# Kernel tuning notes

Measured on AMD Instinct MI355X. Metric: run time of the kernel, lower is better.

The kernel has to match this reference:

```python
import jax, jax.numpy as jnp
import numpy as np

WS = 7           # window size
N = WS * WS      # tokens per window = 49
C = 128          # embed dim
H = 4            # heads
HD = C // H      # head dim = 32
NW = 64          # num windows (mask leading dim)
B = 4096         # total windows = outer_batch * NW


def _relative_indexes():
    ch = np.arange(WS)
    cw = np.arange(WS)
    coords = np.stack(np.meshgrid(ch, cw, indexing='ij')).reshape(2, -1)  # [2, N]
    rel = coords[:, :, None] - coords[:, None, :]                          # [2, N, N]
    rel = rel.transpose(1, 2, 0)
    rel[:, :, 0] += WS - 1
    rel[:, :, 1] += WS - 1
    rel[:, :, 0] *= 2 * WS - 1
    return jnp.asarray(rel.sum(-1), dtype=jnp.int32)                       # [N, N]


def setup_inputs() -> dict:
    key = jax.random.key(0)
    ks = jax.random.split(key, 10)
    s = 0.02
    return {
        'query': jax.random.normal(ks[0], (B, N, C), jnp.float32),
        'source': jax.random.normal(ks[1], (B, N, C), jnp.float32),
        'mask': jnp.zeros((NW, N, N), jnp.float32),
        'q_w': jax.random.normal(ks[2], (C, C), jnp.float32) * s,
        'q_b': jnp.zeros((C,), jnp.float32),
        'kv_w': jax.random.normal(ks[3], (C, 2 * C), jnp.float32) * s,
        'kv_b': jnp.zeros((2 * C,), jnp.float32),
        'proj_w': jax.random.normal(ks[4], (C, C), jnp.float32) * s,
        'proj_b': jnp.zeros((C,), jnp.float32),
        'bias_table': jax.random.normal(ks[5], ((2 * WS - 1) ** 2, H), jnp.float32) * s,
        'rel_idx': _relative_indexes(),
    }


def reference(query, source, mask, q_w, q_b, kv_w, kv_b, proj_w, proj_b, bias_table, rel_idx):
    scale = HD ** -0.5
    q = query @ q_w + q_b                       # [B, N, C]
    kv = source @ kv_w + kv_b                   # [B, N, 2C]
    k, v = kv[..., :C], kv[..., C:]
    # [B, N, H, HD] -> [B, H, N, HD]
    q = q.reshape(B, N, H, HD).transpose(0, 2, 1, 3) * scale
    k = k.reshape(B, N, H, HD).transpose(0, 2, 1, 3)
    v = v.reshape(B, N, H, HD).transpose(0, 2, 1, 3)
    attn = jnp.einsum('bhnd,bhmd->bhnm', q, k)  # [B, H, N, N]
    # gathered relative positional bias: [1, H, N, N]
    bias = bias_table[rel_idx.reshape(-1)].reshape(N, N, H).transpose(2, 0, 1)[None]
    attn = attn + bias
    # mask: [NW, N, N] broadcast over outer batch and heads
    attn = attn.reshape(-1, NW, H, N, N) + mask[None, :, None]
    attn = attn.reshape(B, H, N, N)
    attn = jax.nn.softmax(attn, axis=-1)
    x = jnp.einsum('bhnm,bhmd->bnhd', attn, v).reshape(B, N, C)
    return x @ proj_w + proj_b
```

## Files before the change

kernel.cpp:

```cpp
#include <hip/hip_runtime.h>
#include <hip/hip_bf16.h>

#define NN 49
#define CC 128
#define HH 4
#define NWIN 64
#define BB 4096
#define QSCALE 0.17677669529663687f

typedef __attribute__((ext_vector_type(8))) short bf16x8;
typedef __attribute__((ext_vector_type(4))) float f32x4;
typedef unsigned short u16;
typedef unsigned int u32;

__device__ __forceinline__ u16 f2b(float f) {
    __hip_bfloat16 h = __float2bfloat16(f);
    return __builtin_bit_cast(u16, h);
}
__device__ __forceinline__ float b2f(u16 u) { return __uint_as_float(((u32)u) << 16); }
__device__ __forceinline__ uint2 pack4(float a, float b, float c, float d) {
    uint2 r;
    r.x = (u32)f2b(a) | ((u32)f2b(b) << 16);
    r.y = (u32)f2b(c) | ((u32)f2b(d) << 16);
    return r;
}
__device__ __forceinline__ f32x4 mfma16(bf16x8 a, bf16x8 b, f32x4 c) {
    return __builtin_amdgcn_mfma_f32_16x16x32_bf16(a, b, c, 0, 0, 0);
}
__device__ __forceinline__ char* adr256(u16* base, int row, int byte) {
    return (char*)base + row * 256 + (byte ^ ((row & 7) << 4));
}
__device__ __forceinline__ char* adr128(u16* base, int row, int byte) {
    return (char*)base + row * 128 + (byte ^ ((row & 7) << 4));
}

__global__ void prep_cbt(const float* __restrict__ bias_table, const int* __restrict__ rel_idx,
                         const float* __restrict__ mask, u16* __restrict__ cbt) {
    int idx = blockIdx.x * blockDim.x + threadIdx.x;
    int m = idx & 63, i = (idx >> 6) & 63, h = (idx >> 12) & 3, wv = idx >> 14;
    if (wv >= NWIN) return;
    float v = -1e9f;
    if (m < NN && i < NN)
        v = bias_table[rel_idx[i * NN + m] * HH + h] + mask[(wv * NN + i) * NN + m];
    cbt[idx] = f2b(v);
}

__global__ void prep_w(const float* __restrict__ qw, const float* __restrict__ qb,
                       const float* __restrict__ kvw, const float* __restrict__ pjw,
                       u16* __restrict__ qwp, u16* __restrict__ kvwp,
                       u16* __restrict__ pjwp, float* __restrict__ qbs) {
    int idx = blockIdx.x * blockDim.x + threadIdx.x;
    if (idx < 16384) {
        int i = idx & 7, lane = (idx >> 3) & 63, kt = (idx >> 9) & 3, nt = idx >> 11;
        int k = 32 * kt + 8 * (lane >> 4) + i, n = 16 * nt + (lane & 15);
        qwp[idx] = f2b(qw[k * CC + n] * QSCALE);
    } else if (idx < 49152) {
        int j = idx - 16384;
        int i = j & 7, lane = (j >> 3) & 63, kt = (j >> 9) & 3, nt = j >> 11;
        int k = 32 * kt + 8 * (lane >> 4) + i, n = 16 * nt + (lane & 15);
        kvwp[j] = f2b(kvw[k * 2 * CC + n]);
    } else if (idx < 65536) {
        int j = idx - 49152;
        int i = j & 7, lane = (j >> 3) & 63, kt = (j >> 9) & 3, nt = j >> 11;
        int k = 32 * kt + 8 * (lane >> 4) + i, n = 16 * nt + (lane & 15);
        pjwp[j] = f2b(pjw[k * CC + n]);
    } else if (idx < 65664) {
        int j = idx - 65536;
        qbs[j] = qb[j] * QSCALE;
    }
}

__global__ __launch_bounds__(512, 4)
void wmha_main(const float* __restrict__ query, const float* __restrict__ source,
               const u16* __restrict__ qwp, const u16* __restrict__ kvwp,
               const u16* __restrict__ pjwp, const float* __restrict__ qbs,
               const float* __restrict__ kv_b, const float* __restrict__ proj_b,
               const u16* __restrict__ cbt, float* __restrict__ out) {
    __shared__ u16 lds[24576];
    u16* R0 = lds;
    u16* R1 = lds + 8192;
    u16* R2 = lds + 16384;
    const int t = threadIdx.x;
    const int b = blockIdx.x;
    const int w = t >> 6, lane = t & 63;
    const int lq = lane & 15, qd = lane >> 4;
    const int mw = w >> 2;
    const int nw = w & 3;
    const int h = w >> 1;
    const int half = w & 1;

    {
        const int row = t >> 3, qu = t & 7;
        const size_t gbase = (size_t)b * NN * CC + row * CC + qu * 8;
        #pragma unroll
        for (int j = 0; j < 2; ++j) {
            bf16x8 vq = {0,0,0,0,0,0,0,0}, vs = {0,0,0,0,0,0,0,0};
            if (row < NN) {
                const float4* q4 = (const float4*)(query + gbase) + 16 * j;
                const float4* s4 = (const float4*)(source + gbase) + 16 * j;
                float4 a0 = q4[0], a1 = q4[1], c0 = s4[0], c1 = s4[1];
                vq[0]=(short)f2b(a0.x); vq[1]=(short)f2b(a0.y); vq[2]=(short)f2b(a0.z); vq[3]=(short)f2b(a0.w);
                vq[4]=(short)f2b(a1.x); vq[5]=(short)f2b(a1.y); vq[6]=(short)f2b(a1.z); vq[7]=(short)f2b(a1.w);
                vs[0]=(short)f2b(c0.x); vs[1]=(short)f2b(c0.y); vs[2]=(short)f2b(c0.z); vs[3]=(short)f2b(c0.w);
                vs[4]=(short)f2b(c1.x); vs[5]=(short)f2b(c1.y); vs[6]=(short)f2b(c1.z); vs[7]=(short)f2b(c1.w);
            }
            *(bf16x8*)adr256(R0, row, qu * 16 + 128 * j) = vq;
            *(bf16x8*)adr256(R2, row, qu * 16 + 128 * j) = vs;
        }
    }
    bf16x8 bwq[2][4];
    #pragma unroll
    for (int n2 = 0; n2 < 2; ++n2)
        #pragma unroll
        for (int kt = 0; kt < 4; ++kt)
            bwq[n2][kt] = *(const bf16x8*)(qwp + (((nw + 4 * n2) * 4 + kt) * 64 + lane) * 8);
    __syncthreads();

    {
        bf16x8 a[2][4];
        #pragma unroll
        for (int m2 = 0; m2 < 2; ++m2)
            #pragma unroll
            for (int kt = 0; kt < 4; ++kt)
                a[m2][kt] = *(const bf16x8*)adr256(R0, (2 * mw + m2) * 16 + lq, kt * 64 + qd * 16);
        f32x4 acc[2][2] = {};
        __builtin_amdgcn_s_setprio(1);
        #pragma unroll
        for (int m2 = 0; m2 < 2; ++m2)
            #pragma unroll
            for (int n2 = 0; n2 < 2; ++n2)
                #pragma unroll
                for (int kt = 0; kt < 4; ++kt)
                    acc[m2][n2] = mfma16(a[m2][kt], bwq[n2][kt], acc[m2][n2]);
        __builtin_amdgcn_s_setprio(0);
        #pragma unroll
        for (int n2 = 0; n2 < 2; ++n2) {
            const int col = 16 * (nw + 4 * n2) + lq;
            const float bias = qbs[col];
            #pragma unroll
            for (int m2 = 0; m2 < 2; ++m2)
                #pragma unroll
                for (int r = 0; r < 4; ++r) {
                    const int row = (2 * mw + m2) * 16 + qd * 4 + r;
                    *(u16*)adr256(R1, row, 2 * col) = f2b(acc[m2][n2][r] + bias);
                }
        }
    }
    __syncthreads();

    {
        bf16x8 bw[2][4];
        #pragma unroll
        for (int n2 = 0; n2 < 2; ++n2)
            #pragma unroll
            for (int kt = 0; kt < 4; ++kt)
                bw[n2][kt] = *(const bf16x8*)(kvwp + (((nw + 4 * n2) * 4 + kt) * 64 + lane) * 8);
        bf16x8 a[2][4];
        #pragma unroll
        for (int m2 = 0; m2 < 2; ++m2)
            #pragma unroll
            for (int kt = 0; kt < 4; ++kt)
                a[m2][kt] = *(const bf16x8*)adr256(R2, (2 * mw + m2) * 16 + lq, kt * 64 + qd * 16);
        f32x4 acc[2][2] = {};
        __builtin_amdgcn_s_setprio(1);
        #pragma unroll
        for (int m2 = 0; m2 < 2; ++m2)
            #pragma unroll
            for (int n2 = 0; n2 < 2; ++n2)
                #pragma unroll
                for (int kt = 0; kt < 4; ++kt)
                    acc[m2][n2] = mfma16(a[m2][kt], bw[n2][kt], acc[m2][n2]);
        __builtin_amdgcn_s_setprio(0);
        #pragma unroll
        for (int n2 = 0; n2 < 2; ++n2) {
            const int col = 16 * (nw + 4 * n2) + lq;
            const float bias = kv_b[col];
            #pragma unroll
            for (int m2 = 0; m2 < 2; ++m2)
                #pragma unroll
                for (int r = 0; r < 4; ++r) {
                    const int row = (2 * mw + m2) * 16 + qd * 4 + r;
                    *(u16*)adr256(R0, row, 2 * col) = f2b(acc[m2][n2][r] + bias);
                }
        }
    }

    {
        bf16x8 bw[2][4];
        #pragma unroll
        for (int n2 = 0; n2 < 2; ++n2)
            #pragma unroll
            for (int kt = 0; kt < 4; ++kt)
                bw[n2][kt] = *(const bf16x8*)(kvwp + (((8 + nw + 4 * n2) * 4 + kt) * 64 + lane) * 8);
        bf16x8 a[2][4];
        #pragma unroll
        for (int m2 = 0; m2 < 2; ++m2)
            #pragma unroll
            for (int kt = 0; kt < 4; ++kt)
                a[m2][kt] = *(const bf16x8*)adr256(R2, (2 * mw + m2) * 16 + lq, kt * 64 + qd * 16);
        f32x4 acc[2][2] = {};
        __builtin_amdgcn_s_setprio(1);
        #pragma unroll
        for (int m2 = 0; m2 < 2; ++m2)
            #pragma unroll
            for (int n2 = 0; n2 < 2; ++n2)
                #pragma unroll
                for (int kt = 0; kt < 4; ++kt)
                    acc[m2][n2] = mfma16(a[m2][kt], bw[n2][kt], acc[m2][n2]);
        __builtin_amdgcn_s_setprio(0);
        __syncthreads();
        #pragma unroll
        for (int n2 = 0; n2 < 2; ++n2) {
            const int dim = 16 * (nw + 4 * n2) + lq;
            const float bias = kv_b[CC + dim];
            #pragma unroll
            for (int m2 = 0; m2 < 2; ++m2) {
                uint2 pk = pack4(acc[m2][n2][0] + bias, acc[m2][n2][1] + bias,
                                 acc[m2][n2][2] + bias, acc[m2][n2][3] + bias);
                *(uint2*)adr128(R2, dim, 2 * ((2 * mw + m2) * 16 + qd * 4)) = pk;
            }
        }
    }

    f32x4 s[2][4];
    {
        bf16x8 kf[4], qf[2];
        #pragma unroll
        for (int a = 0; a < 4; ++a)
            kf[a] = *(const bf16x8*)adr256(R0, a * 16 + lq, h * 64 + qd * 16);
        #pragma unroll
        for (int i = 0; i < 2; ++i)
            qf[i] = *(const bf16x8*)adr256(R1, (2 * half + i) * 16 + lq, h * 64 + qd * 16);
        __builtin_amdgcn_s_setprio(1);
        #pragma unroll
        for (int i = 0; i < 2; ++i) {
            f32x4 z = {0.f, 0.f, 0.f, 0.f};
            #pragma unroll
            for (int a = 0; a < 4; ++a)
                s[i][a] = mfma16(kf[a], qf[i], z);
        }
        __builtin_amdgcn_s_setprio(0);
    }
    __syncthreads();

    {
        bf16x8 vf[2][2];
        #pragma unroll
        for (int dt = 0; dt < 2; ++dt)
            #pragma unroll
            for (int kt = 0; kt < 2; ++kt)
                vf[dt][kt] = *(const bf16x8*)adr128(R2, h * 32 + dt * 16 + lq, kt * 64 + qd * 16);
        u16* pb = R0 + w * 1024;
        const u16* cbb = cbt + ((size_t)((b & (NWIN - 1)) * HH + h) << 12);
        #pragma unroll
        for (int i = 0; i < 2; ++i) {
            const int bq = 2 * half + i;
            uint2 cb2[4];
            #pragma unroll
            for (int a = 0; a < 4; ++a)
                cb2[a] = *(const uint2*)(cbb + (bq * 16 + lq) * 64 + a * 16 + qd * 4);
            #pragma unroll
            for (int a = 0; a < 4; ++a) {
                s[i][a][0] += b2f((u16)(cb2[a].x & 0xffffu));
                s[i][a][1] += b2f((u16)(cb2[a].x >> 16));
                s[i][a][2] += b2f((u16)(cb2[a].y & 0xffffu));
                s[i][a][3] += b2f((u16)(cb2[a].y >> 16));
            }
            float m0 = s[i][0][0];
            #pragma unroll
            for (int a = 0; a < 4; ++a)
                #pragma unroll
                for (int r = 0; r < 4; ++r) m0 = fmaxf(m0, s[i][a][r]);
            m0 = fmaxf(m0, __shfl_xor(m0, 16));
            m0 = fmaxf(m0, __shfl_xor(m0, 32));
            uint2 pk[4];
            float sm = 0.f;
            #pragma unroll
            for (int a = 0; a < 4; ++a) {
                float p0 = __expf(s[i][a][0] - m0), p1 = __expf(s[i][a][1] - m0);
                float p2 = __expf(s[i][a][2] - m0), p3 = __expf(s[i][a][3] - m0);
                pk[a] = pack4(p0, p1, p2, p3);
                sm += b2f((u16)pk[a].x) + b2f((u16)(pk[a].x >> 16))
                    + b2f((u16)pk[a].y) + b2f((u16)(pk[a].y >> 16));
            }
            sm += __shfl_xor(sm, 16);
            sm += __shfl_xor(sm, 32);
            const float inv = 1.f / sm;
            #pragma unroll
            for (int a = 0; a < 4; ++a)
                *(uint2*)adr128(pb, lq, 32 * a + 8 * qd) = pk[a];
            asm volatile("s_waitcnt lgkmcnt(0)" ::: "memory");
            __builtin_amdgcn_sched_barrier(0);
            f32x4 o[2] = {{0.f,0.f,0.f,0.f},{0.f,0.f,0.f,0.f}};
            __builtin_amdgcn_s_setprio(1);
            #pragma unroll
            for (int kt = 0; kt < 2; ++kt) {
                bf16x8 pf = *(const bf16x8*)adr128(pb, lq, 64 * kt + 16 * qd);
                #pragma unroll
                for (int dt = 0; dt < 2; ++dt)
                    o[dt] = mfma16(vf[dt][kt], pf, o[dt]);
            }
            __builtin_amdgcn_s_setprio(0);
            __builtin_amdgcn_sched_barrier(0);
            #pragma unroll
            for (int dt = 0; dt < 2; ++dt) {
                uint2 px = pack4(o[dt][0] * inv, o[dt][1] * inv,
                                 o[dt][2] * inv, o[dt][3] * inv);
                *(uint2*)adr256(R1, bq * 16 + lq, 64 * h + 32 * dt + 8 * qd) = px;
            }
        }
    }

    {
        bf16x8 bw[2][4];
        #pragma unroll
        for (int n2 = 0; n2 < 2; ++n2)
            #pragma unroll
            for (int kt = 0; kt < 4; ++kt)
                bw[n2][kt] = *(const bf16x8*)(pjwp + (((nw + 4 * n2) * 4 + kt) * 64 + lane) * 8);
        __syncthreads();
        bf16x8 a[2][4];
        #pragma unroll
        for (int m2 = 0; m2 < 2; ++m2)
            #pragma unroll
            for (int kt = 0; kt < 4; ++kt)
                a[m2][kt] = *(const bf16x8*)adr256(R1, (2 * mw + m2) * 16 + lq, kt * 64 + qd * 16);
        f32x4 acc[2][2] = {};
        __builtin_amdgcn_s_setprio(1);
        #pragma unroll
        for (int m2 = 0; m2 < 2; ++m2)
            #pragma unroll
            for (int n2 = 0; n2 < 2; ++n2)
                #pragma unroll
                for (int kt = 0; kt < 4; ++kt)
                    acc[m2][n2] = mfma16(a[m2][kt], bw[n2][kt], acc[m2][n2]);
        __builtin_amdgcn_s_setprio(0);
        float* outb = out + (size_t)b * NN * CC;
        #pragma unroll
        for (int n2 = 0; n2 < 2; ++n2) {
            const int col = 16 * (nw + 4 * n2) + lq;
            const float bias = proj_b[col];
            #pragma unroll
            for (int m2 = 0; m2 < 2; ++m2)
                #pragma unroll
                for (int r = 0; r < 4; ++r) {
                    const int row = (2 * mw + m2) * 16 + qd * 4 + r;
                    if (row < NN) outb[row * CC + col] = acc[m2][n2][r] + bias;
                }
        }
    }
}

extern "C" void kernel_launch(void* const* d_in, const int* in_sizes, int n_in,
                              void* d_out, int out_size, void* d_ws, size_t ws_size,
                              hipStream_t stream) {
    const float* query      = (const float*)d_in[0];
    const float* source     = (const float*)d_in[1];
    const float* mask       = (const float*)d_in[2];
    const float* q_w        = (const float*)d_in[3];
    const float* q_b        = (const float*)d_in[4];
    const float* kv_w       = (const float*)d_in[5];
    const float* kv_b       = (const float*)d_in[6];
    const float* proj_w     = (const float*)d_in[7];
    const float* proj_b     = (const float*)d_in[8];
    const float* bias_table = (const float*)d_in[9];
    const int*   rel_idx    = (const int*)d_in[10];
    float* out = (float*)d_out;

    u16* cbt   = (u16*)d_ws;
    u16* qwp   = cbt + 1048576;
    u16* kvwp  = qwp + 16384;
    u16* pjwp  = kvwp + 32768;
    float* qbs = (float*)(pjwp + 16384);

    prep_cbt<<<4096, 256, 0, stream>>>(bias_table, rel_idx, mask, cbt);
    prep_w<<<257, 256, 0, stream>>>(q_w, q_b, kv_w, proj_w, qwp, kvwp, pjwp, qbs);
    wmha_main<<<BB, 512, 0, stream>>>(query, source, qwp, kvwp, pjwp, qbs,
                                      kv_b, proj_b, cbt, out);
}
```

Before: 130.1 us.

## Load activations directly into MFMA registers and swap operands for vectorized stores

Query and source rows now go straight from global memory into bf16 MFMA operand registers instead of being staged through LDS. This removes the staging writes and reads and two of the three block barriers. Q, K and the output projection swap their MFMA operands so each lane holds four consecutive columns, which allows 8-byte LDS stores and 16-byte float4 global output stores in place of scalar ones. The cost is uncoalesced, strided per-lane global reads of the inputs and higher register pressure from holding the source fragments across the K and V GEMMs.

```diff
diff --git a/kernel.cpp b/kernel.cpp
--- a/kernel.cpp
+++ b/kernel.cpp
@@ -33,6 +33,15 @@
 __device__ __forceinline__ char* adr128(u16* base, int row, int byte) {
     return (char*)base + row * 128 + (byte ^ ((row & 7) << 4));
 }
+__device__ __forceinline__ bf16x8 ldcvt(const float* p) {
+    float4 x0 = ((const float4*)p)[0];
+    float4 x1 = ((const float4*)p)[1];
+    bf16x8 v;
+    v[0]=(short)f2b(x0.x); v[1]=(short)f2b(x0.y); v[2]=(short)f2b(x0.z); v[3]=(short)f2b(x0.w);
+    v[4]=(short)f2b(x1.x); v[5]=(short)f2b(x1.y); v[6]=(short)f2b(x1.z); v[7]=(short)f2b(x1.w);
+    return v;
+}
+__device__ __forceinline__ bf16x8 zero8() { bf16x8 v = {0,0,0,0,0,0,0,0}; return v; }
 
 __global__ void prep_cbt(const float* __restrict__ bias_table, const int* __restrict__ rel_idx,
                          const float* __restrict__ mask, u16* __restrict__ cbt) {
@@ -77,9 +86,9 @@
                const float* __restrict__ kv_b, const float* __restrict__ proj_b,
                const u16* __restrict__ cbt, float* __restrict__ out) {
     __shared__ u16 lds[24576];
-    u16* R0 = lds;
-    u16* R1 = lds + 8192;
-    u16* R2 = lds + 16384;
+    u16* Q  = lds;
+    u16* K  = lds + 8192;
+    u16* VT = lds + 16384;
     const int t = threadIdx.x;
     const int b = blockIdx.x;
     const int w = t >> 6, lane = t & 63;
@@ -89,148 +98,128 @@
     const int h = w >> 1;
     const int half = w & 1;
 
-    {
-        const int row = t >> 3, qu = t & 7;
-        const size_t gbase = (size_t)b * NN * CC + row * CC + qu * 8;
-        #pragma unroll
-        for (int j = 0; j < 2; ++j) {
-            bf16x8 vq = {0,0,0,0,0,0,0,0}, vs = {0,0,0,0,0,0,0,0};
-            if (row < NN) {
-                const float4* q4 = (const float4*)(query + gbase) + 16 * j;
-                const float4* s4 = (const float4*)(source + gbase) + 16 * j;
-                float4 a0 = q4[0], a1 = q4[1], c0 = s4[0], c1 = s4[1];
-                vq[0]=(short)f2b(a0.x); vq[1]=(short)f2b(a0.y); vq[2]=(short)f2b(a0.z); vq[3]=(short)f2b(a0.w);
-                vq[4]=(short)f2b(a1.x); vq[5]=(short)f2b(a1.y); vq[6]=(short)f2b(a1.z); vq[7]=(short)f2b(a1.w);
-                vs[0]=(short)f2b(c0.x); vs[1]=(short)f2b(c0.y); vs[2]=(short)f2b(c0.z); vs[3]=(short)f2b(c0.w);
-                vs[4]=(short)f2b(c1.x); vs[5]=(short)f2b(c1.y); vs[6]=(short)f2b(c1.z); vs[7]=(short)f2b(c1.w);
-            }
-            *(bf16x8*)adr256(R0, row, qu * 16 + 128 * j) = vq;
-            *(bf16x8*)adr256(R2, row, qu * 16 + 128 * j) = vs;
-        }
-    }
-    bf16x8 bwq[2][4];
-    #pragma unroll
-    for (int n2 = 0; n2 < 2; ++n2)
-        #pragma unroll
-        for (int kt = 0; kt < 4; ++kt)
-            bwq[n2][kt] = *(const bf16x8*)(qwp + (((nw + 4 * n2) * 4 + kt) * 64 + lane) * 8);
+    const float* xq = query  + (size_t)b * NN * CC;
+    const float* xs = source + (size_t)b * NN * CC;
+
+    {
+        bf16x8 bwq[2][4];
+        #pragma unroll
+        for (int n2 = 0; n2 < 2; ++n2)
+            #pragma unroll
+            for (int kt = 0; kt < 4; ++kt)
+                bwq[n2][kt] = *(const bf16x8*)(qwp + (((nw + 4 * n2) * 4 + kt) * 64 + lane) * 8);
+        f32x4 acc[2][2] = {};
+        #pragma unroll
+        for (int m2 = 0; m2 < 2; ++m2) {
+            const int tok = (2 * mw + m2) * 16 + lq;
+            const float* xr = xq + tok * CC + qd * 8;
+            bf16x8 a[4];
+            #pragma unroll
+            for (int kt = 0; kt < 4; ++kt)
+                a[kt] = (tok < NN) ? ldcvt(xr + kt * 32) : zero8();
+            __builtin_amdgcn_s_setprio(1);
+            #pragma unroll
+            for (int n2 = 0; n2 < 2; ++n2)
+                #pragma unroll
+                for (int kt = 0; kt < 4; ++kt)
+                    acc[m2][n2] = mfma16(bwq[n2][kt], a[kt], acc[m2][n2]);
+            __builtin_amdgcn_s_setprio(0);
+        }
+        #pragma unroll
+        for (int n2 = 0; n2 < 2; ++n2) {
+            const int cb0 = 16 * (nw + 4 * n2) + 4 * qd;
+            const float4 bia = *(const float4*)(qbs + cb0);
+            #pragma unroll
+            for (int m2 = 0; m2 < 2; ++m2) {
+                const int tok = (2 * mw + m2) * 16 + lq;
+                uint2 pk = pack4(acc[m2][n2][0] + bia.x, acc[m2][n2][1] + bia.y,
+                                 acc[m2][n2][2] + bia.z, acc[m2][n2][3] + bia.w);
+                *(uint2*)adr256(Q, tok, 2 * cb0) = pk;
+            }
+        }
+    }
+
+    {
+        bf16x8 as[2][4];
+        #pragma unroll
+        for (int m2 = 0; m2 < 2; ++m2) {
+            const int tok = (2 * mw + m2) * 16 + lq;
+            const float* xr = xs + tok * CC + qd * 8;
+            #pragma unroll
+            for (int kt = 0; kt < 4; ++kt)
+                as[m2][kt] = (tok < NN) ? ldcvt(xr + kt * 32) : zero8();
+        }
+        {
+            bf16x8 bwk[2][4];
+            #pragma unroll
+            for (int n2 = 0; n2 < 2; ++n2)
+                #pragma unroll
+                for (int kt = 0; kt < 4; ++kt)
+                    bwk[n2][kt] = *(const bf16x8*)(kvwp + (((nw + 4 * n2) * 4 + kt) * 64 + lane) * 8);
+            f32x4 acc[2][2] = {};
+            __builtin_amdgcn_s_setprio(1);
+            #pragma unroll
+            for (int m2 = 0; m2 < 2; ++m2)
+                #pragma unroll
+                for (int n2 = 0; n2 < 2; ++n2)
+                    #pragma unroll
+                    for (int kt = 0; kt < 4; ++kt)
+                        acc[m2][n2] = mfma16(bwk[n2][kt], as[m2][kt], acc[m2][n2]);
+            __builtin_amdgcn_s_setprio(0);
+            #pragma unroll
+            for (int n2 = 0; n2 < 2; ++n2) {
+                const int cb0 = 16 * (nw + 4 * n2) + 4 * qd;
+                const float4 bia = *(const float4*)(kv_b + cb0);
+                #pragma unroll
+                for (int m2 = 0; m2 < 2; ++m2) {
+                    const int tok = (2 * mw + m2) * 16 + lq;
+                    uint2 pk = pack4(acc[m2][n2][0] + bia.x, acc[m2][n2][1] + bia.y,
+                                     acc[m2][n2][2] + bia.z, acc[m2][n2][3] + bia.w);
+                    *(uint2*)adr256(K, tok, 2 * cb0) = pk;
+                }
+            }
+        }
+        {
+            bf16x8 bwv[2][4];
+            #pragma unroll
+            for (int n2 = 0; n2 < 2; ++n2)
+                #pragma unroll
+                for (int kt = 0; kt < 4; ++kt)
+                    bwv[n2][kt] = *(const bf16x8*)(kvwp + (((8 + nw + 4 * n2) * 4 + kt) * 64 + lane) * 8);
+            f32x4 acc[2][2] = {};
+            __builtin_amdgcn_s_setprio(1);
+            #pragma unroll
+            for (int m2 = 0; m2 < 2; ++m2)
+                #pragma unroll
+                for (int n2 = 0; n2 < 2; ++n2)
+                    #pragma unroll
+                    for (int kt = 0; kt < 4; ++kt)
+                        acc[m2][n2] = mfma16(as[m2][kt], bwv[n2][kt], acc[m2][n2]);
+            __builtin_amdgcn_s_setprio(0);
+            #pragma unroll
+            for (int n2 = 0; n2 < 2; ++n2) {
+                const int dim = 16 * (nw + 4 * n2) + lq;
+                const float bias = kv_b[CC + dim];
+                #pragma unroll
+                for (int m2 = 0; m2 < 2; ++m2) {
+                    uint2 pk = pack4(acc[m2][n2][0] + bias, acc[m2][n2][1] + bias,
+                                     acc[m2][n2][2] + bias, acc[m2][n2][3] + bias);
+                    *(uint2*)adr128(VT, dim, 2 * ((2 * mw + m2) * 16 + qd * 4)) = pk;
+                }
+            }
+        }
+    }
     __syncthreads();
 
-    {
-        bf16x8 a[2][4];
-        #pragma unroll
-        for (int m2 = 0; m2 < 2; ++m2)
-            #pragma unroll
-            for (int kt = 0; kt < 4; ++kt)
-                a[m2][kt] = *(const bf16x8*)adr256(R0, (2 * mw + m2) * 16 + lq, kt * 64 + qd * 16);
-        f32x4 acc[2][2] = {};
-        __builtin_amdgcn_s_setprio(1);
-        #pragma unroll
-        for (int m2 = 0; m2 < 2; ++m2)
-            #pragma unroll
-            for (int n2 = 0; n2 < 2; ++n2)
-                #pragma unroll
-                for (int kt = 0; kt < 4; ++kt)
-                    acc[m2][n2] = mfma16(a[m2][kt], bwq[n2][kt], acc[m2][n2]);
-        __builtin_amdgcn_s_setprio(0);
-        #pragma unroll
-        for (int n2 = 0; n2 < 2; ++n2) {
-            const int col = 16 * (nw + 4 * n2) + lq;
-            const float bias = qbs[col];
-            #pragma unroll
-            for (int m2 = 0; m2 < 2; ++m2)
-                #pragma unroll
-                for (int r = 0; r < 4; ++r) {
-                    const int row = (2 * mw + m2) * 16 + qd * 4 + r;
-                    *(u16*)adr256(R1, row, 2 * col) = f2b(acc[m2][n2][r] + bias);
-                }
-        }
-    }
-    __syncthreads();
-
-    {
-        bf16x8 bw[2][4];
-        #pragma unroll
-        for (int n2 = 0; n2 < 2; ++n2)
-            #pragma unroll
-            for (int kt = 0; kt < 4; ++kt)
-                bw[n2][kt] = *(const bf16x8*)(kvwp + (((nw + 4 * n2) * 4 + kt) * 64 + lane) * 8);
-        bf16x8 a[2][4];
-        #pragma unroll
-        for (int m2 = 0; m2 < 2; ++m2)
-            #pragma unroll
-            for (int kt = 0; kt < 4; ++kt)
-                a[m2][kt] = *(const bf16x8*)adr256(R2, (2 * mw + m2) * 16 + lq, kt * 64 + qd * 16);
-        f32x4 acc[2][2] = {};
-        __builtin_amdgcn_s_setprio(1);
-        #pragma unroll
-        for (int m2 = 0; m2 < 2; ++m2)
-            #pragma unroll
-            for (int n2 = 0; n2 < 2; ++n2)
-                #pragma unroll
-                for (int kt = 0; kt < 4; ++kt)
-                    acc[m2][n2] = mfma16(a[m2][kt], bw[n2][kt], acc[m2][n2]);
-        __builtin_amdgcn_s_setprio(0);
-        #pragma unroll
-        for (int n2 = 0; n2 < 2; ++n2) {
-            const int col = 16 * (nw + 4 * n2) + lq;
-            const float bias = kv_b[col];
-            #pragma unroll
-            for (int m2 = 0; m2 < 2; ++m2)
-                #pragma unroll
-                for (int r = 0; r < 4; ++r) {
-                    const int row = (2 * mw + m2) * 16 + qd * 4 + r;
-                    *(u16*)adr256(R0, row, 2 * col) = f2b(acc[m2][n2][r] + bias);
-                }
-        }
-    }
-
-    {
-        bf16x8 bw[2][4];
-        #pragma unroll
-        for (int n2 = 0; n2 < 2; ++n2)
-            #pragma unroll
-            for (int kt = 0; kt < 4; ++kt)
-                bw[n2][kt] = *(const bf16x8*)(kvwp + (((8 + nw + 4 * n2) * 4 + kt) * 64 + lane) * 8);
-        bf16x8 a[2][4];
-        #pragma unroll
-        for (int m2 = 0; m2 < 2; ++m2)
-            #pragma unroll
-            for (int kt = 0; kt < 4; ++kt)
-                a[m2][kt] = *(const bf16x8*)adr256(R2, (2 * mw + m2) * 16 + lq, kt * 64 + qd * 16);
-        f32x4 acc[2][2] = {};
-        __builtin_amdgcn_s_setprio(1);
-        #pragma unroll
-        for (int m2 = 0; m2 < 2; ++m2)
-            #pragma unroll
-            for (int n2 = 0; n2 < 2; ++n2)
-                #pragma unroll
-                for (int kt = 0; kt < 4; ++kt)
-                    acc[m2][n2] = mfma16(a[m2][kt], bw[n2][kt], acc[m2][n2]);
-        __builtin_amdgcn_s_setprio(0);
-        __syncthreads();
-        #pragma unroll
-        for (int n2 = 0; n2 < 2; ++n2) {
-            const int dim = 16 * (nw + 4 * n2) + lq;
-            const float bias = kv_b[CC + dim];
-            #pragma unroll
-            for (int m2 = 0; m2 < 2; ++m2) {
-                uint2 pk = pack4(acc[m2][n2][0] + bias, acc[m2][n2][1] + bias,
-                                 acc[m2][n2][2] + bias, acc[m2][n2][3] + bias);
-                *(uint2*)adr128(R2, dim, 2 * ((2 * mw + m2) * 16 + qd * 4)) = pk;
-            }
-        }
-    }
-
     f32x4 s[2][4];
     {
         bf16x8 kf[4], qf[2];
         #pragma unroll
         for (int a = 0; a < 4; ++a)
-            kf[a] = *(const bf16x8*)adr256(R0, a * 16 + lq, h * 64 + qd * 16);
+            kf[a] = *(const bf16x8*)adr256(K, a * 16 + lq, h * 64 + qd * 16);
         #pragma unroll
         for (int i = 0; i < 2; ++i)
-            qf[i] = *(const bf16x8*)adr256(R1, (2 * half + i) * 16 + lq, h * 64 + qd * 16);
+            qf[i] = *(const bf16x8*)adr256(Q, (2 * half + i) * 16 + lq, h * 64 + qd * 16);
         __builtin_amdgcn_s_setprio(1);
         #pragma unroll
         for (int i = 0; i < 2; ++i) {
@@ -249,8 +238,8 @@
         for (int dt = 0; dt < 2; ++dt)
             #pragma unroll
             for (int kt = 0; kt < 2; ++kt)
-                vf[dt][kt] = *(const bf16x8*)adr128(R2, h * 32 + dt * 16 + lq, kt * 64 + qd * 16);
-        u16* pb = R0 + w * 1024;
+                vf[dt][kt] = *(const bf16x8*)adr128(VT, h * 32 + dt * 16 + lq, kt * 64 + qd * 16);
+        u16* pb = Q + w * 1024;
         const u16* cbb = cbt + ((size_t)((b & (NWIN - 1)) * HH + h) << 12);
         #pragma unroll
         for (int i = 0; i < 2; ++i) {
@@ -306,7 +295,7 @@
             for (int dt = 0; dt < 2; ++dt) {
                 uint2 px = pack4(o[dt][0] * inv, o[dt][1] * inv,
                                  o[dt][2] * inv, o[dt][3] * inv);
-                *(uint2*)adr256(R1, bq * 16 + lq, 64 * h + 32 * dt + 8 * qd) = px;
+                *(uint2*)adr256(K, bq * 16 + lq, 64 * h + 32 * dt + 8 * qd) = px;
             }
         }
     }
@@ -324,7 +313,7 @@
         for (int m2 = 0; m2 < 2; ++m2)
             #pragma unroll
             for (int kt = 0; kt < 4; ++kt)
-                a[m2][kt] = *(const bf16x8*)adr256(R1, (2 * mw + m2) * 16 + lq, kt * 64 + qd * 16);
+                a[m2][kt] = *(const bf16x8*)adr256(K, (2 * mw + m2) * 16 + lq, kt * 64 + qd * 16);
         f32x4 acc[2][2] = {};
         __builtin_amdgcn_s_setprio(1);
         #pragma unroll
@@ -333,20 +322,25 @@
             for (int n2 = 0; n2 < 2; ++n2)
                 #pragma unroll
                 for (int kt = 0; kt < 4; ++kt)
-                    acc[m2][n2] = mfma16(a[m2][kt], bw[n2][kt], acc[m2][n2]);
+                    acc[m2][n2] = mfma16(bw[n2][kt], a[m2][kt], acc[m2][n2]);
         __builtin_amdgcn_s_setprio(0);
         float* outb = out + (size_t)b * NN * CC;
         #pragma unroll
         for (int n2 = 0; n2 < 2; ++n2) {
-            const int col = 16 * (nw + 4 * n2) + lq;
-            const float bias = proj_b[col];
-            #pragma unroll
-            for (int m2 = 0; m2 < 2; ++m2)
-                #pragma unroll
-                for (int r = 0; r < 4; ++r) {
-                    const int row = (2 * mw + m2) * 16 + qd * 4 + r;
-                    if (row < NN) outb[row * CC + col] = acc[m2][n2][r] + bias;
+            const int cb0 = 16 * (nw + 4 * n2) + 4 * qd;
+            const float4 bia = *(const float4*)(proj_b + cb0);
+            #pragma unroll
+            for (int m2 = 0; m2 < 2; ++m2) {
+                const int tok = (2 * mw + m2) * 16 + lq;
+                if (tok < NN) {
+                    float4 vst;
+                    vst.x = acc[m2][n2][0] + bia.x;
+                    vst.y = acc[m2][n2][1] + bia.y;
+                    vst.z = acc[m2][n2][2] + bia.z;
+                    vst.w = acc[m2][n2][3] + bia.w;
+                    *(float4*)(outb + tok * CC + cb0) = vst;
                 }
+            }
         }
     }
 }
```

Measured after the change: 206.6 us. 58.8% more time.
